# Optimization experiments

Measured on AMD Instinct MI355X. Metric: run time of the kernel, lower is better.

The kernel has to match this reference:

```python
import jax, jax.numpy as jnp
import numpy as np

N = 65536   # total nodes
B = 128     # graphs
G = 512     # nodes per graph
E = 65536   # directed edges (before BU flip + self loops)
IN = 512    # in_feats
HID = 64    # hid_feats
OUT = 64    # out_feats
H = 4       # heads (self.K)
NC = 4      # num_class


def _gat(x, src, dst, W, a_src, a_dst, bias, heads, out_ch, concat):
    # PyG GATConv: lin (no bias) -> per-edge LeakyReLU(0.2) attention logits ->
    # softmax over edges grouped by destination -> weighted sum -> +bias.
    n = x.shape[0]
    h = (x @ W).reshape(n, heads, out_ch)            # [N,H,C]
    asrc = (h * a_src).sum(-1)                       # [N,H]
    adst = (h * a_dst).sum(-1)                       # [N,H]
    e = jax.nn.leaky_relu(asrc[src] + adst[dst], 0.2)  # [Etot,H]
    m = jax.ops.segment_max(e, dst, num_segments=n)
    m = jnp.where(jnp.isfinite(m), m, 0.0)
    ex = jnp.exp(e - m[dst])
    den = jax.ops.segment_sum(ex, dst, num_segments=n)
    alpha = ex / den[dst]                            # self-loops guarantee den>0
    out = jax.ops.segment_sum(alpha[:, :, None] * h[src], dst, num_segments=n)
    out = out.reshape(n, heads * out_ch) if concat else out.mean(1)
    return out + bias


def _smean(v, seg, nseg):
    s = jax.ops.segment_sum(v, seg, num_segments=nseg)
    c = jax.ops.segment_sum(jnp.ones((v.shape[0], 1), v.dtype), seg, num_segments=nseg)
    return s / jnp.maximum(c, 1.0)


def setup_inputs() -> dict:
    key = jax.random.key(0)
    ks = jax.random.split(key, 24)
    x = jax.random.normal(ks[0], (N, IN), jnp.float32)
    root = jax.random.normal(ks[1], (B, IN), jnp.float32)
    # edges kept within each graph of G contiguous nodes (PyG batching layout)
    gid = jax.random.randint(ks[2], (E,), 0, B)
    src = gid * G + jax.random.randint(ks[3], (E,), 0, G)
    dst = gid * G + jax.random.randint(ks[4], (E,), 0, G)
    edge_index = jnp.stack([src, dst]).astype(jnp.int32)
    batch = jnp.repeat(jnp.arange(B, dtype=jnp.int32), G)
    ptr = jnp.arange(B + 1, dtype=jnp.int32) * G
    s = 0.05
    r = lambda i, shp: jax.random.normal(ks[i], shp, jnp.float32) * s
    return {
        'x': x, 'root': root, 'edge_index': edge_index, 'batch': batch, 'ptr': ptr,
        'W_post1': r(5, (IN, HID)), 'W_claim1': r(6, (IN, HID)),
        'W1': r(7, (2 * HID, H * HID)), 'att_src1': r(8, (H, HID)),
        'att_dst1': r(9, (H, HID)), 'b1': r(10, (H * HID,)),
        'W_post2': r(11, (HID, HID)), 'W_claim2': r(12, (IN, HID)),
        'W2': r(13, (8 * HID, H * OUT)), 'att_src2': r(14, (H, OUT)),
        'att_dst2': r(15, (H, OUT)), 'b2': r(16, (OUT,)),
        'W_fc': r(17, (4 * OUT, OUT)), 'b_fc': r(18, (OUT,)),
        'W_clf': r(19, (2 * OUT, NC)), 'b_clf': r(20, (NC,)),
    }


def reference(x, root, edge_index, batch, ptr,
              W_post1, W_claim1, W1, att_src1, att_dst1, b1,
              W_post2, W_claim2, W2, att_src2, att_dst2, b2,
              W_fc, b_fc, W_clf, b_clf):
    n = x.shape[0]
    nb = root.shape[0]
    # merged edges: TD + BU (flipped), then self loops (add_self_loops=True)
    merged = jnp.concatenate([edge_index, edge_index[::-1]], axis=1)
    loops = jnp.arange(n, dtype=edge_index.dtype)
    ei = jnp.concatenate([merged, jnp.stack([loops, loops])], axis=1)
    src, dst = ei[0], ei[1]
    # root broadcast (replaces per-batch python loop)
    root_extend = root[batch]                         # [N,IN]
    # PostLevelAttention: gated fusion of node feats and root feats
    h_x = x @ W_post1
    h_c = root_extend @ W_claim1
    g = jax.nn.sigmoid(h_x + h_c)
    h1 = jnp.concatenate([g * h_x + (1 - g) * h_c, h_x], -1)   # [N,2*HID]
    x2 = _gat(h1, src, dst, W1, att_src1, att_dst1, b1, H, HID, True)  # [N,4*HID]
    xr = jax.nn.relu(x2)
    # PostLevelAttention2 on each of the K=4 head slices (vectorized over k)
    hs = jnp.einsum('nkh,hd->nkd', xr.reshape(n, H, HID), W_post2)  # [N,4,HID]
    hc2 = (root_extend @ W_claim2)[:, None, :]                      # [N,1,HID]
    g2 = jax.nn.sigmoid(hs + hc2)
    x3 = jnp.concatenate([g2 * hs + (1 - g2) * hc2, hs], -1).reshape(n, 8 * HID)
    x4 = _gat(x3, src, dst, W2, att_src2, att_dst2, b2, H, OUT, False)  # [N,OUT]
    xr2 = jax.nn.relu(x4)
    # root embedding per graph (x[ptr[i]]) broadcast back to nodes
    h_c3 = xr2[ptr[:-1]][batch]                        # [N,OUT]
    h_joint = jnp.concatenate([h_c3, xr2, xr2 * h_c3, jnp.abs(h_c3 - xr2)], 1)
    beta = jax.nn.softmax(jnp.tanh(h_joint @ W_fc + b_fc), axis=-1)
    s_hat = _smean(beta * xr2, batch, nb)
    s = _smean(xr2, batch, nb)
    logits = jnp.concatenate([s_hat, s], 1) @ W_clf + b_clf
    return jax.nn.log_softmax(logits, axis=1)
```

## Files before the change

kernel.cpp:

```cpp
#include <hip/hip_runtime.h>
#include <math.h>

#define NN   65536
#define BB   128
#define GGR  512
#define EE   65536
#define INF_ 512
#define HIDD 64

typedef __attribute__((ext_vector_type(8))) short bf16x8;
typedef __attribute__((ext_vector_type(4))) float f32x4;
typedef unsigned short ushort_t;
typedef unsigned int uint_t;

static __device__ __forceinline__ float sigmoidf_(float x){ return 1.0f/(1.0f+__expf(-x)); }
static __device__ __forceinline__ float lrelu_(float x){ return x>=0.0f ? x : 0.2f*x; }
static __device__ __forceinline__ float tanhf_(float x){
  float e = __expf(2.f*x);
  return 1.f - 2.f/(e + 1.f);
}

static __device__ __forceinline__ ushort_t f2b(float f){
  union { float f; uint_t u; } v; v.f = f;
  uint_t u = v.u;
  uint_t r = (u + 0x7fffu + ((u >> 16) & 1u)) >> 16;
  return (ushort_t)r;
}
static __device__ __forceinline__ float b2f(uint_t u16){
  union { uint_t u; float f; } v; v.u = u16 << 16; return v.f;
}

__global__ void k_prep(const float* __restrict__ W1, const float* __restrict__ W2,
                       const float* __restrict__ Wp1, const float* __restrict__ Wp2,
                       const float* __restrict__ Wfc,
                       ushort_t* __restrict__ W1t, ushort_t* __restrict__ W2t,
                       ushort_t* __restrict__ Wp1t, ushort_t* __restrict__ Wp2t,
                       ushort_t* __restrict__ Wfct,
                       const float* __restrict__ root, const float* __restrict__ Wc1,
                       const float* __restrict__ Wc2, float* __restrict__ hc1,
                       float* __restrict__ hc2){
  if (blockIdx.x >= 832){
    int b = blockIdx.x - 832;
    int f = threadIdx.x;
    if (f < 64){
      const float* r = root + (size_t)b*INF_;
      float a1 = 0.f, a2 = 0.f;
      for (int k = 0; k < INF_; ++k){
        float rv = r[k];
        a1 = fmaf(rv, Wc1[k*HIDD+f], a1);
        a2 = fmaf(rv, Wc2[k*HIDD+f], a2);
      }
      hc1[b*HIDD+f] = a1; hc2[b*HIDD+f] = a2;
    }
    return;
  }
  int idx = blockIdx.x*256 + threadIdx.x;
  if (idx < 32768){
    int k = idx >> 8, c = idx & 255;
    W1t[(size_t)c*128 + k] = f2b(W1[idx]);
  } else if (idx < 163840){
    int j = idx - 32768; int k = j >> 8, c = j & 255;
    W2t[(size_t)c*512 + k] = f2b(W2[j]);
  } else if (idx < 196608){
    int j = idx - 163840; int k = j >> 6, c = j & 63;
    Wp1t[(size_t)c*512 + k] = f2b(Wp1[j]);
  } else if (idx < 200704){
    int j = idx - 196608; int k = j >> 6, c = j & 63;
    Wp2t[(size_t)c*64 + k] = f2b(Wp2[j]);
  } else if (idx < 212992){
    int j = idx - 200704; int k = j >> 6, c = j & 63;
    Wfct[(size_t)c*192 + k] = f2b(Wfc[4096 + j]);
  }
}

__global__ __launch_bounds__(256) void k_l1(
    const float* __restrict__ x,
    const ushort_t* __restrict__ Wp1t,
    const float* __restrict__ hc1,
    const ushort_t* __restrict__ W1t,
    const float* __restrict__ att_s, const float* __restrict__ att_d,
    ushort_t* __restrict__ Hout,
    float* __restrict__ asrc, float* __restrict__ adst){
  __shared__ __align__(16) char Hc[16384];
  int tid = threadIdx.x;
  int w = tid >> 6, lane = tid & 63;
  int lr = lane & 15, lk = lane >> 4;
  int n0 = blockIdx.x * 64;
  int g = n0 >> 9;
  int sw = (lr & 7) << 4;
  f32x4 accA[4];
  #pragma unroll
  for (int ci = 0; ci < 4; ++ci) accA[ci] = (f32x4){0.f,0.f,0.f,0.f};
  const char* xrow = (const char*)x + (size_t)(n0 + w*16 + lr)*2048 + lk*32;
  const ushort_t* BbA = Wp1t + (size_t)lr*512 + lk*8;
  #pragma unroll
  for (int j = 0; j < 16; ++j){
    float4 a0 = *(const float4*)(xrow + j*128);
    float4 a1 = *(const float4*)(xrow + j*128 + 16);
    bf16x8 af;
    af[0]=(short)f2b(a0.x); af[1]=(short)f2b(a0.y); af[2]=(short)f2b(a0.z); af[3]=(short)f2b(a0.w);
    af[4]=(short)f2b(a1.x); af[5]=(short)f2b(a1.y); af[6]=(short)f2b(a1.z); af[7]=(short)f2b(a1.w);
    #pragma unroll
    for (int ci = 0; ci < 4; ++ci){
      bf16x8 bfv = *(const bf16x8*)(BbA + (size_t)ci*16*512 + j*32);
      accA[ci] = __builtin_amdgcn_mfma_f32_16x16x32_bf16(af, bfv, accA[ci], 0, 0, 0);
    }
  }
  #pragma unroll
  for (int ci = 0; ci < 4; ++ci){
    int col = ci*16 + lr;
    float hc = hc1[g*64 + col];
    #pragma unroll
    for (int q = 0; q < 4; ++q){
      int row = w*16 + lk*4 + q;
      int swr = (row & 7) << 4;
      float hx = accA[ci][q];
      float gg = sigmoidf_(hx + hc);
      float fo = gg*hx + (1.f-gg)*hc;
      *(ushort_t*)(Hc + ((row*256 + col*2) ^ swr))        = f2b(fo);
      *(ushort_t*)(Hc + ((row*256 + (64 + col)*2) ^ swr)) = f2b(hx);
    }
  }
  __syncthreads();
  int c0 = w * 64;
  f32x4 acc[4][4];
  #pragma unroll
  for (int ri = 0; ri < 4; ++ri)
    #pragma unroll
    for (int ci = 0; ci < 4; ++ci) acc[ri][ci] = (f32x4){0.f,0.f,0.f,0.f};
  #pragma unroll
  for (int k0 = 0; k0 < 128; k0 += 32){
    bf16x8 af[4], bfv[4];
    #pragma unroll
    for (int ri = 0; ri < 4; ++ri){
      int lg = (ri*16 + lr)*256 + (k0 + lk*8)*2;
      af[ri] = *(const bf16x8*)(Hc + (lg ^ sw));
    }
    #pragma unroll
    for (int ci = 0; ci < 4; ++ci)
      bfv[ci] = *(const bf16x8*)(W1t + (size_t)(c0 + ci*16 + lr)*128 + k0 + lk*8);
    #pragma unroll
    for (int ri = 0; ri < 4; ++ri)
      #pragma unroll
      for (int ci = 0; ci < 4; ++ci)
        acc[ri][ci] = __builtin_amdgcn_mfma_f32_16x16x32_bf16(af[ri], bfv[ci], acc[ri][ci], 0, 0, 0);
  }
  float as_[4], ad_[4];
  #pragma unroll
  for (int ci = 0; ci < 4; ++ci){
    as_[ci] = att_s[c0 + ci*16 + lr];
    ad_[ci] = att_d[c0 + ci*16 + lr];
  }
  #pragma unroll
  for (int ri = 0; ri < 4; ++ri){
    #pragma unroll
    for (int q = 0; q < 4; ++q){
      int row = n0 + ri*16 + lk*4 + q;
      float ps = 0.f, pd = 0.f;
      #pragma unroll
      for (int ci = 0; ci < 4; ++ci){
        float v = acc[ri][ci][q];
        Hout[(size_t)row*256 + c0 + ci*16 + lr] = f2b(v);
        ps = fmaf(v, as_[ci], ps);
        pd = fmaf(v, ad_[ci], pd);
      }
      #pragma unroll
      for (int m = 1; m < 16; m <<= 1){
        ps += __shfl_xor(ps, m);
        pd += __shfl_xor(pd, m);
      }
      if (lr == 0){
        asrc[(size_t)row*4 + w] = ps;
        adst[(size_t)row*4 + w] = pd;
      }
    }
  }
}

__global__ __launch_bounds__(256) void k_l2(
    const ushort_t* __restrict__ xrb,
    const ushort_t* __restrict__ Wp2t,
    const float* __restrict__ hc2,
    const ushort_t* __restrict__ W2t,
    const float* __restrict__ att_s, const float* __restrict__ att_d,
    ushort_t* __restrict__ Hout,
    float* __restrict__ asrc, float* __restrict__ adst){
  __shared__ __align__(16) ushort_t x3s[64*128];
  int tid = threadIdx.x;
  int w = tid >> 6, lane = tid & 63;
  int lr = lane & 15, lk = lane >> 4;
  int n0 = blockIdx.x * 64;
  int g = n0 >> 9;
  int sw = (lr & 7) << 4;
  char* Sc = (char*)x3s;
  const ushort_t* Ab = xrb + (size_t)(n0 + w*16 + lr)*256 + lk*8;
  int c0 = w * 64;
  f32x4 acc[4][4];
  #pragma unroll
  for (int ri = 0; ri < 4; ++ri)
    #pragma unroll
    for (int ci = 0; ci < 4; ++ci) acc[ri][ci] = (f32x4){0.f,0.f,0.f,0.f};
  for (int hd = 0; hd < 4; ++hd){
    f32x4 acc2[4];
    #pragma unroll
    for (int ci = 0; ci < 4; ++ci) acc2[ci] = (f32x4){0.f,0.f,0.f,0.f};
    #pragma unroll
    for (int k0 = 0; k0 < 64; k0 += 32){
      bf16x8 af = *(const bf16x8*)(Ab + hd*64 + k0);
      #pragma unroll
      for (int ci = 0; ci < 4; ++ci){
        bf16x8 bfv = *(const bf16x8*)(Wp2t + (size_t)(ci*16 + lr)*64 + k0 + lk*8);
        acc2[ci] = __builtin_amdgcn_mfma_f32_16x16x32_bf16(af, bfv, acc2[ci], 0, 0, 0);
      }
    }
    #pragma unroll
    for (int ci = 0; ci < 4; ++ci){
      int col = ci*16 + lr;
      float hc = hc2[g*64 + col];
      #pragma unroll
      for (int q = 0; q < 4; ++q){
        int row = w*16 + lk*4 + q;
        int swr = (row & 7) << 4;
        float a = acc2[ci][q];
        float gg = sigmoidf_(a + hc);
        *(ushort_t*)(Sc + ((row*256 + col*2) ^ swr))        = f2b(gg*a + (1.f-gg)*hc);
        *(ushort_t*)(Sc + ((row*256 + (64 + col)*2) ^ swr)) = f2b(a);
      }
    }
    __syncthreads();
    #pragma unroll
    for (int k0 = 0; k0 < 128; k0 += 32){
      bf16x8 af[4], bfv[4];
      #pragma unroll
      for (int ri = 0; ri < 4; ++ri){
        int lg = (ri*16 + lr)*256 + (k0 + lk*8)*2;
        af[ri] = *(const bf16x8*)(Sc + (lg ^ sw));
      }
      #pragma unroll
      for (int ci = 0; ci < 4; ++ci)
        bfv[ci] = *(const bf16x8*)(W2t + (size_t)(c0 + ci*16 + lr)*512 + hd*128 + k0 + lk*8);
      #pragma unroll
      for (int ri = 0; ri < 4; ++ri)
        #pragma unroll
        for (int ci = 0; ci < 4; ++ci)
          acc[ri][ci] = __builtin_amdgcn_mfma_f32_16x16x32_bf16(af[ri], bfv[ci], acc[ri][ci], 0, 0, 0);
    }
    if (hd < 3) __syncthreads();
  }
  float as_[4], ad_[4];
  #pragma unroll
  for (int ci = 0; ci < 4; ++ci){
    as_[ci] = att_s[c0 + ci*16 + lr];
    ad_[ci] = att_d[c0 + ci*16 + lr];
  }
  #pragma unroll
  for (int ri = 0; ri < 4; ++ri){
    #pragma unroll
    for (int q = 0; q < 4; ++q){
      int row = n0 + ri*16 + lk*4 + q;
      float ps = 0.f, pd = 0.f;
      #pragma unroll
      for (int ci = 0; ci < 4; ++ci){
        float v = acc[ri][ci][q];
        Hout[(size_t)row*256 + c0 + ci*16 + lr] = f2b(v);
        ps = fmaf(v, as_[ci], ps);
        pd = fmaf(v, ad_[ci], pd);
      }
      #pragma unroll
      for (int m = 1; m < 16; m <<= 1){
        ps += __shfl_xor(ps, m);
        pd += __shfl_xor(pd, m);
      }
      if (lr == 0){
        asrc[(size_t)row*4 + w] = ps;
        adst[(size_t)row*4 + w] = pd;
      }
    }
  }
}

__global__ void k_count(const int* __restrict__ ei, int* __restrict__ deg){
  int t = blockIdx.x*256 + threadIdx.x;
  int s = ei[t], d = ei[EE + t];
  atomicAdd(&deg[d], 1);
  atomicAdd(&deg[s], 1);
}

__global__ void k_scan1(const int* __restrict__ deg, int* __restrict__ offa,
                        int* __restrict__ bsum){
  __shared__ int sm[256];
  int tid = threadIdx.x, idx = blockIdx.x*256 + tid;
  int v = deg[idx] + 1;
  sm[tid] = v; __syncthreads();
  for (int o = 1; o < 256; o <<= 1){
    int t = (tid >= o) ? sm[tid-o] : 0;
    __syncthreads();
    sm[tid] += t;
    __syncthreads();
  }
  offa[idx] = sm[tid] - v;
  if (tid == 255) bsum[blockIdx.x] = sm[255];
}

__global__ void k_scan2(int* __restrict__ bsum){
  __shared__ int sm[256];
  int tid = threadIdx.x;
  int v = bsum[tid];
  sm[tid] = v; __syncthreads();
  for (int o = 1; o < 256; o <<= 1){
    int t = (tid >= o) ? sm[tid-o] : 0;
    __syncthreads();
    sm[tid] += t;
    __syncthreads();
  }
  bsum[tid] = sm[tid] - v;
}

__global__ void k_scan3(int* __restrict__ offa, const int* __restrict__ bsum){
  int idx = blockIdx.x*256 + threadIdx.x;
  offa[idx] += bsum[idx >> 8];
}

__global__ void k_fill(const int* __restrict__ ei, const int* __restrict__ offa,
                       int* __restrict__ cur, int* __restrict__ elist){
  int t = blockIdx.x*256 + threadIdx.x;
  int s = ei[t], d = ei[EE + t];
  int p = atomicAdd(&cur[d], 1); elist[offa[d] + p] = s;
  p = atomicAdd(&cur[s], 1);     elist[offa[s] + p] = d;
  p = atomicAdd(&cur[t], 1);     elist[offa[t] + p] = t;
}

template<int LAYER>
__global__ __launch_bounds__(256) void k_agg(const int* __restrict__ offa,
                                             const int* __restrict__ deg,
                                             const int* __restrict__ elist,
                                             const ushort_t* __restrict__ h,
                                             const float* __restrict__ asrc,
                                             const float* __restrict__ adst,
                                             const float* __restrict__ bias,
                                             ushort_t* __restrict__ outb,
                                             float* __restrict__ outf){
  __shared__ float eS[4][4][17][4];
  __shared__ int   sS[4][4][17];
  int bid = blockIdx.x;
  int swz = (bid & 7) * (4096/8) + (bid >> 3);
  int tid = threadIdx.x;
  int wave = tid >> 6, lane = tid & 63;
  int grp = lane >> 4, l = lane & 15;
  int n = swz*16 + wave*4 + grp;
  int o0 = offa[n], cnt = deg[n] + 1;
  float4 adv = *(const float4*)&adst[(size_t)n*4];
  float ad[4] = {adv.x, adv.y, adv.z, adv.w};
  int lim = (cnt < 16) ? cnt : 16;
  int s_l = elist[o0 + ((l < cnt) ? l : 0)];
  float4 asv = *(const float4*)&asrc[(size_t)s_l*4];
  float e_l[4];
  e_l[0] = lrelu_(asv.x + ad[0]); e_l[1] = lrelu_(asv.y + ad[1]);
  e_l[2] = lrelu_(asv.z + ad[2]); e_l[3] = lrelu_(asv.w + ad[3]);
  if (l < lim){
    sS[wave][grp][l] = s_l;
    *(float4*)&eS[wave][grp][l][0] = make_float4(e_l[0], e_l[1], e_l[2], e_l[3]);
  }
  float m[4];
  #pragma unroll
  for (int hh = 0; hh < 4; ++hh) m[hh] = (l < cnt) ? e_l[hh] : -1e30f;
  for (int i = 16 + l; i < cnt; i += 16){
    int s = elist[o0 + i];
    float4 a2 = *(const float4*)&asrc[(size_t)s*4];
    m[0] = fmaxf(m[0], lrelu_(a2.x + ad[0]));
    m[1] = fmaxf(m[1], lrelu_(a2.y + ad[1]));
    m[2] = fmaxf(m[2], lrelu_(a2.z + ad[2]));
    m[3] = fmaxf(m[3], lrelu_(a2.w + ad[3]));
  }
  #pragma unroll
  for (int mask = 1; mask < 16; mask <<= 1)
    #pragma unroll
    for (int hh = 0; hh < 4; ++hh) m[hh] = fmaxf(m[hh], __shfl_xor(m[hh], mask));
  int myh = l >> 2;
  float mm = m[myh];
  float den = 0.f;
  float accv[16] = {};
  for (int i = 0; i < lim; ++i){
    int s = sS[wave][grp][i];
    float e = eS[wave][grp][i][myh];
    float ex = __expf(e - mm);
    den += ex;
    const uint4* hp = (const uint4*)(h + (size_t)s*256 + l*16);
    uint4 h0 = hp[0], h1v = hp[1];
    uint_t uu[8] = {h0.x, h0.y, h0.z, h0.w, h1v.x, h1v.y, h1v.z, h1v.w};
    #pragma unroll
    for (int r = 0; r < 8; ++r){
      accv[2*r+0] = fmaf(ex, b2f(uu[r] & 0xffffu), accv[2*r+0]);
      accv[2*r+1] = fmaf(ex, b2f(uu[r] >> 16),     accv[2*r+1]);
    }
  }
  for (int i = 16; i < cnt; ++i){
    int s = elist[o0 + i];
    float4 a2 = *(const float4*)&asrc[(size_t)s*4];
    float e = lrelu_(((const float*)&a2)[myh] + ad[myh]);
    float ex = __expf(e - mm);
    den += ex;
    const uint4* hp = (const uint4*)(h + (size_t)s*256 + l*16);
    uint4 h0 = hp[0], h1v = hp[1];
    uint_t uu[8] = {h0.x, h0.y, h0.z, h0.w, h1v.x, h1v.y, h1v.z, h1v.w};
    #pragma unroll
    for (int r = 0; r < 8; ++r){
      accv[2*r+0] = fmaf(ex, b2f(uu[r] & 0xffffu), accv[2*r+0]);
      accv[2*r+1] = fmaf(ex, b2f(uu[r] >> 16),     accv[2*r+1]);
    }
  }
  float inv = 1.0f / den;
  if (LAYER == 1){
    #pragma unroll
    for (int r = 0; r < 4; ++r){
      int c = l*16 + r*4;
      float4 bv = *(const float4*)&bias[c];
      float o0v = fmaxf(accv[r*4+0]*inv + bv.x, 0.f);
      float o1v = fmaxf(accv[r*4+1]*inv + bv.y, 0.f);
      float o2v = fmaxf(accv[r*4+2]*inv + bv.z, 0.f);
      float o3v = fmaxf(accv[r*4+3]*inv + bv.w, 0.f);
      uint2 pk;
      pk.x = (uint_t)f2b(o0v) | ((uint_t)f2b(o1v) << 16);
      pk.y = (uint_t)f2b(o2v) | ((uint_t)f2b(o3v) << 16);
      *(uint2*)&outb[(size_t)n*256 + c] = pk;
    }
  } else {
    #pragma unroll
    for (int r = 0; r < 16; ++r) accv[r] *= inv;
    #pragma unroll
    for (int r = 0; r < 16; ++r){
      accv[r] += __shfl_xor(accv[r], 4);
      accv[r] += __shfl_xor(accv[r], 8);
    }
    if (l < 4){
      #pragma unroll
      for (int r = 0; r < 4; ++r){
        int c = l*16 + r*4;
        float4 bv = *(const float4*)&bias[c];
        float4 o;
        o.x = fmaxf(accv[r*4+0]*0.25f + bv.x, 0.f);
        o.y = fmaxf(accv[r*4+1]*0.25f + bv.y, 0.f);
        o.z = fmaxf(accv[r*4+2]*0.25f + bv.z, 0.f);
        o.w = fmaxf(accv[r*4+3]*0.25f + bv.w, 0.f);
        *(float4*)&outf[(size_t)n*64 + c] = o;
      }
    }
  }
}

__global__ __launch_bounds__(256) void k_pool_mfma(
    const float* __restrict__ xr2,
    const ushort_t* __restrict__ Wfct,
    const float* __restrict__ Wfc,
    const float* __restrict__ bfc,
    float* __restrict__ shat,
    float* __restrict__ ssum){
  __shared__ __align__(16) float xs[64][68];
  __shared__ float rls[64];
  __shared__ float bs[64];
  __shared__ float ls_sh[64];
  __shared__ float ls_s[64];
  int tid = threadIdx.x;
  int n0 = blockIdx.x * 64;
  int g = n0 >> 9;
  {
    int row = tid >> 4, col4 = (tid & 15) * 4;
    #pragma unroll
    for (int i = 0; i < 4; ++i){
      float4 v = *(const float4*)&xr2[(size_t)(n0 + row + i*16)*64 + col4];
      *(float4*)&xs[row + i*16][col4] = v;
    }
    if (tid < 16){
      float4 v = *(const float4*)&xr2[(size_t)((size_t)g*GGR)*64 + tid*4];
      *(float4*)&rls[tid*4] = v;
    }
    if (tid >= 128 && tid < 192){ ls_sh[tid-128] = 0.f; ls_s[tid-128] = 0.f; }
  }
  __syncthreads();
  if (tid < 64){
    float b = bfc[tid];
    for (int j = 0; j < 64; ++j) b = fmaf(rls[j], Wfc[j*64 + tid], b);
    bs[tid] = b;
  }
  __syncthreads();
  int w = tid >> 6, lane = tid & 63;
  int lr = lane & 15, lk = lane >> 4;
  f32x4 acc[4];
  #pragma unroll
  for (int ci = 0; ci < 4; ++ci) acc[ci] = (f32x4){0.f,0.f,0.f,0.f};
  int arow = w*16 + lr;
  #pragma unroll
  for (int k0 = 0; k0 < 192; k0 += 32){
    int seg = k0 >> 6;
    int cb = (k0 & 63) + lk*8;
    bf16x8 af;
    #pragma unroll
    for (int j = 0; j < 8; ++j){
      float xv = xs[arow][cb + j];
      float rv = rls[cb + j];
      float v = (seg == 0) ? xv : (seg == 1 ? xv*rv : fabsf(rv - xv));
      af[j] = (short)f2b(v);
    }
    #pragma unroll
    for (int ci = 0; ci < 4; ++ci){
      bf16x8 bfv = *(const bf16x8*)(Wfct + (size_t)(ci*16+lr)*192 + k0 + lk*8);
      acc[ci] = __builtin_amdgcn_mfma_f32_16x16x32_bf16(af, bfv, acc[ci], 0, 0, 0);
    }
  }
  float bsv[4];
  #pragma unroll
  for (int ci = 0; ci < 4; ++ci) bsv[ci] = bs[ci*16 + lr];
  float c_sh[4] = {0.f,0.f,0.f,0.f}, c_s[4] = {0.f,0.f,0.f,0.f};
  #pragma unroll
  for (int q = 0; q < 4; ++q){
    int rrow = w*16 + lk*4 + q;
    float t[4];
    float mx = -1e30f;
    #pragma unroll
    for (int ci = 0; ci < 4; ++ci){
      t[ci] = tanhf_(acc[ci][q] + bsv[ci]);
      mx = fmaxf(mx, t[ci]);
    }
    #pragma unroll
    for (int mask = 1; mask < 16; mask <<= 1) mx = fmaxf(mx, __shfl_xor(mx, mask));
    float e[4], s = 0.f;
    #pragma unroll
    for (int ci = 0; ci < 4; ++ci){ e[ci] = __expf(t[ci] - mx); s += e[ci]; }
    #pragma unroll
    for (int mask = 1; mask < 16; mask <<= 1) s += __shfl_xor(s, mask);
    float invs = 1.0f / s;
    #pragma unroll
    for (int ci = 0; ci < 4; ++ci){
      float xv = xs[rrow][ci*16 + lr];
      c_sh[ci] = fmaf(e[ci]*invs, xv, c_sh[ci]);
      c_s[ci] += xv;
    }
  }
  #pragma unroll
  for (int ci = 0; ci < 4; ++ci){
    c_sh[ci] += __shfl_xor(c_sh[ci], 16); c_sh[ci] += __shfl_xor(c_sh[ci], 32);
    c_s[ci]  += __shfl_xor(c_s[ci], 16);  c_s[ci]  += __shfl_xor(c_s[ci], 32);
  }
  if (lk == 0){
    #pragma unroll
    for (int ci = 0; ci < 4; ++ci){
      atomicAdd(&ls_sh[ci*16 + lr], c_sh[ci]);
      atomicAdd(&ls_s[ci*16 + lr], c_s[ci]);
    }
  }
  __syncthreads();
  if (tid < 64){
    atomicAdd(&shat[g*64 + tid], ls_sh[tid]);
    atomicAdd(&ssum[g*64 + tid], ls_s[tid]);
  }
}

__global__ void k_final(const float* __restrict__ shat, const float* __restrict__ ssum,
                        const float* __restrict__ Wc, const float* __restrict__ bc,
                        float* __restrict__ outp){
  int g = threadIdx.x;
  float l0 = bc[0], l1 = bc[1], l2 = bc[2], l3 = bc[3];
  const float s512 = 1.0f/512.0f;
  for (int j = 0; j < 64; ++j){
    float sh = shat[g*64 + j]*s512;
    float ss = ssum[g*64 + j]*s512;
    float4 w1 = *(const float4*)&Wc[j*4];
    float4 w2 = *(const float4*)&Wc[(64+j)*4];
    l0 = fmaf(sh, w1.x, fmaf(ss, w2.x, l0));
    l1 = fmaf(sh, w1.y, fmaf(ss, w2.y, l1));
    l2 = fmaf(sh, w1.z, fmaf(ss, w2.z, l2));
    l3 = fmaf(sh, w1.w, fmaf(ss, w2.w, l3));
  }
  float mx = fmaxf(fmaxf(l0,l1), fmaxf(l2,l3));
  float s = __expf(l0-mx)+__expf(l1-mx)+__expf(l2-mx)+__expf(l3-mx);
  float lse = mx + logf(s);
  outp[g*4+0] = l0 - lse;
  outp[g*4+1] = l1 - lse;
  outp[g*4+2] = l2 - lse;
  outp[g*4+3] = l3 - lse;
}

extern "C" void kernel_launch(void* const* d_in, const int* in_sizes, int n_in,
                              void* d_out, int out_size, void* d_ws, size_t ws_size,
                              hipStream_t stream){
  const float* x        = (const float*)d_in[0];
  const float* root     = (const float*)d_in[1];
  const int*   ei       = (const int*)d_in[2];
  const float* W_post1  = (const float*)d_in[5];
  const float* W_claim1 = (const float*)d_in[6];
  const float* W1       = (const float*)d_in[7];
  const float* att_src1 = (const float*)d_in[8];
  const float* att_dst1 = (const float*)d_in[9];
  const float* b1       = (const float*)d_in[10];
  const float* W_post2  = (const float*)d_in[11];
  const float* W_claim2 = (const float*)d_in[12];
  const float* W2       = (const float*)d_in[13];
  const float* att_src2 = (const float*)d_in[14];
  const float* att_dst2 = (const float*)d_in[15];
  const float* b2       = (const float*)d_in[16];
  const float* W_fc     = (const float*)d_in[17];
  const float* b_fc     = (const float*)d_in[18];
  const float* W_clf    = (const float*)d_in[19];
  const float* b_clf    = (const float*)d_in[20];
  float* out = (float*)d_out;

  char* w = (char*)d_ws;
  size_t o = 0;
  auto alloc = [&](size_t bytes)->char*{ char* p = w + o; o += (bytes + 255) & ~(size_t)255; return p; };
  ushort_t* RB   = (ushort_t*)alloc((size_t)NN*256*2);
  ushort_t* xrb  = (ushort_t*)alloc((size_t)NN*256*2);
  float* xr2  = (float*)alloc((size_t)NN*64*4);
  float* asrc = (float*)alloc((size_t)NN*4*4);
  float* adst = (float*)alloc((size_t)NN*4*4);
  float* hc1  = (float*)alloc(128*64*4);
  float* hc2  = (float*)alloc(128*64*4);
  ushort_t* W1t  = (ushort_t*)alloc((size_t)256*128*2);
  ushort_t* W2t  = (ushort_t*)alloc((size_t)256*512*2);
  ushort_t* Wp1t = (ushort_t*)alloc((size_t)64*512*2);
  ushort_t* Wp2t = (ushort_t*)alloc((size_t)64*64*2);
  ushort_t* Wfct = (ushort_t*)alloc((size_t)64*192*2);
  int*   deg  = (int*)alloc((size_t)NN*4);
  int*   cur  = (int*)alloc((size_t)NN*4);
  int*   offa = (int*)alloc((size_t)NN*4);
  int*   bsum = (int*)alloc(256*4);
  int*   elist= (int*)alloc((size_t)(2*EE+NN)*4);
  float* shat = (float*)alloc(128*64*4);
  float* ssumv= (float*)alloc(128*64*4);

  ushort_t* h2b = RB;
  ushort_t* h3b = RB;

  hipMemsetAsync(deg,  0, (size_t)NN*8, stream);
  hipMemsetAsync(shat, 0, 2*128*64*4, stream);

  k_prep<<<960, 256, 0, stream>>>(W1, W2, W_post1, W_post2, W_fc,
                                  W1t, W2t, Wp1t, Wp2t, Wfct,
                                  root, W_claim1, W_claim2, hc1, hc2);
  k_count<<<256, 256, 0, stream>>>(ei, deg);
  k_scan1<<<256, 256, 0, stream>>>(deg, offa, bsum);
  k_scan2<<<1, 256, 0, stream>>>(bsum);
  k_scan3<<<256, 256, 0, stream>>>(offa, bsum);
  k_fill<<<256, 256, 0, stream>>>(ei, offa, cur, elist);
  k_l1<<<1024, 256, 0, stream>>>(x, Wp1t, hc1, W1t, att_src1, att_dst1, h2b, asrc, adst);
  k_agg<1><<<4096, 256, 0, stream>>>(offa, deg, elist, h2b, asrc, adst, b1, xrb, nullptr);
  k_l2<<<1024, 256, 0, stream>>>(xrb, Wp2t, hc2, W2t, att_src2, att_dst2, h3b, asrc, adst);
  k_agg<2><<<4096, 256, 0, stream>>>(offa, deg, elist, h3b, asrc, adst, b2, nullptr, xr2);
  k_pool_mfma<<<1024, 256, 0, stream>>>(xr2, Wfct, W_fc, b_fc, shat, ssumv);
  k_final<<<1, 128, 0, stream>>>(shat, ssumv, W_clf, b_clf, out);
  (void)in_sizes; (void)n_in; (void)out_size; (void)ws_size;
}
```

Measured before the change: 245.3 us.

## Fuse layer-1 GAT aggregation into layer-2 projection kernel via shared memory

The layer-1 attention aggregation (softmax over incoming edges plus bias and ReLU) now runs inside the layer-2 GEMM kernel. Each block aggregates its 64 nodes into a swizzled LDS tile and feeds that tile straight to the MFMA projections, so the 32 MB bf16 xrb intermediate is never written to or read back from global memory, and one launch disappears. Separate buffers for h2/h3 and the layer-2 attention scalars are added so the fused kernel can read layer-1 data while writing layer-2 outputs. In exchange, the fused kernel uses about 48 KB of LDS per block, which can lower occupancy, and only 1024 blocks now do the gather work that was previously spread over 4096.

New measurement: 291.0 us. +18.6%, slower.

```diff
diff --git a/kernel.cpp b/kernel.cpp
--- a/kernel.cpp
+++ b/kernel.cpp
@@ -177,24 +177,114 @@
   }
 }
 
-__global__ __launch_bounds__(256) void k_l2(
-    const ushort_t* __restrict__ xrb,
+__global__ __launch_bounds__(256) void k_al2(
+    const int* __restrict__ offa, const int* __restrict__ deg,
+    const int* __restrict__ elist,
+    const ushort_t* __restrict__ h,
+    const float* __restrict__ asrc1, const float* __restrict__ adst1,
+    const float* __restrict__ b1,
     const ushort_t* __restrict__ Wp2t,
     const float* __restrict__ hc2,
     const ushort_t* __restrict__ W2t,
     const float* __restrict__ att_s, const float* __restrict__ att_d,
     ushort_t* __restrict__ Hout,
-    float* __restrict__ asrc, float* __restrict__ adst){
-  __shared__ __align__(16) ushort_t x3s[64*128];
+    float* __restrict__ asrc2, float* __restrict__ adst2){
+  __shared__ __align__(16) char Xs[32768];
+  __shared__ __align__(16) char Sc[16384];
+  float* eS = (float*)Sc;
+  int*   sS = (int*)(Sc + 8192);
   int tid = threadIdx.x;
-  int w = tid >> 6, lane = tid & 63;
+  int bid = blockIdx.x;
+  int swzb = (bid & 7) * 128 + (bid >> 3);
+  int n0 = swzb * 64;
+  int g = n0 >> 9;
+  int wv = tid >> 6, lane = tid & 63;
+  int grp = lane >> 4, l = lane & 15;
   int lr = lane & 15, lk = lane >> 4;
-  int n0 = blockIdx.x * 64;
-  int g = n0 >> 9;
   int sw = (lr & 7) << 4;
-  char* Sc = (char*)x3s;
-  const ushort_t* Ab = xrb + (size_t)(n0 + w*16 + lr)*256 + lk*8;
-  int c0 = w * 64;
+  for (int it = 0; it < 4; ++it){
+    int row = wv*16 + it*4 + grp;
+    int n = n0 + row;
+    int o0 = offa[n], cnt = deg[n] + 1;
+    float4 adv = *(const float4*)&adst1[(size_t)n*4];
+    float ad[4] = {adv.x, adv.y, adv.z, adv.w};
+    int lim = (cnt < 16) ? cnt : 16;
+    int s_l = elist[o0 + ((l < cnt) ? l : 0)];
+    float4 asv = *(const float4*)&asrc1[(size_t)s_l*4];
+    float e_l[4];
+    e_l[0] = lrelu_(asv.x + ad[0]); e_l[1] = lrelu_(asv.y + ad[1]);
+    e_l[2] = lrelu_(asv.z + ad[2]); e_l[3] = lrelu_(asv.w + ad[3]);
+    int slot = wv*4 + grp;
+    if (l < lim){
+      sS[slot*17 + l] = s_l;
+      *(float4*)&eS[(slot*17 + l)*4] = make_float4(e_l[0], e_l[1], e_l[2], e_l[3]);
+    }
+    float m[4];
+    #pragma unroll
+    for (int hh = 0; hh < 4; ++hh) m[hh] = (l < cnt) ? e_l[hh] : -1e30f;
+    for (int i = 16 + l; i < cnt; i += 16){
+      int s = elist[o0 + i];
+      float4 a2 = *(const float4*)&asrc1[(size_t)s*4];
+      m[0] = fmaxf(m[0], lrelu_(a2.x + ad[0]));
+      m[1] = fmaxf(m[1], lrelu_(a2.y + ad[1]));
+      m[2] = fmaxf(m[2], lrelu_(a2.z + ad[2]));
+      m[3] = fmaxf(m[3], lrelu_(a2.w + ad[3]));
+    }
+    #pragma unroll
+    for (int mask = 1; mask < 16; mask <<= 1)
+      #pragma unroll
+      for (int hh = 0; hh < 4; ++hh) m[hh] = fmaxf(m[hh], __shfl_xor(m[hh], mask));
+    int myh = l >> 2;
+    float mm = m[myh];
+    float den = 0.f;
+    float accv[16] = {};
+    for (int i = 0; i < lim; ++i){
+      int s = sS[slot*17 + i];
+      float e = eS[(slot*17 + i)*4 + myh];
+      float ex = __expf(e - mm);
+      den += ex;
+      const uint4* hp = (const uint4*)(h + (size_t)s*256 + l*16);
+      uint4 h0 = hp[0], h1v = hp[1];
+      uint_t uu[8] = {h0.x, h0.y, h0.z, h0.w, h1v.x, h1v.y, h1v.z, h1v.w};
+      #pragma unroll
+      for (int r = 0; r < 8; ++r){
+        accv[2*r+0] = fmaf(ex, b2f(uu[r] & 0xffffu), accv[2*r+0]);
+        accv[2*r+1] = fmaf(ex, b2f(uu[r] >> 16),     accv[2*r+1]);
+      }
+    }
+    for (int i = 16; i < cnt; ++i){
+      int s = elist[o0 + i];
+      float4 a2 = *(const float4*)&asrc1[(size_t)s*4];
+      float e = lrelu_(((const float*)&a2)[myh] + ad[myh]);
+      float ex = __expf(e - mm);
+      den += ex;
+      const uint4* hp = (const uint4*)(h + (size_t)s*256 + l*16);
+      uint4 h0 = hp[0], h1v = hp[1];
+      uint_t uu[8] = {h0.x, h0.y, h0.z, h0.w, h1v.x, h1v.y, h1v.z, h1v.w};
+      #pragma unroll
+      for (int r = 0; r < 8; ++r){
+        accv[2*r+0] = fmaf(ex, b2f(uu[r] & 0xffffu), accv[2*r+0]);
+        accv[2*r+1] = fmaf(ex, b2f(uu[r] >> 16),     accv[2*r+1]);
+      }
+    }
+    float inv = 1.0f / den;
+    int swr = (row & 7) << 4;
+    #pragma unroll
+    for (int r = 0; r < 4; ++r){
+      int c = l*16 + r*4;
+      float4 bv = *(const float4*)&b1[c];
+      float o0v = fmaxf(accv[r*4+0]*inv + bv.x, 0.f);
+      float o1v = fmaxf(accv[r*4+1]*inv + bv.y, 0.f);
+      float o2v = fmaxf(accv[r*4+2]*inv + bv.z, 0.f);
+      float o3v = fmaxf(accv[r*4+3]*inv + bv.w, 0.f);
+      uint2 pk;
+      pk.x = (uint_t)f2b(o0v) | ((uint_t)f2b(o1v) << 16);
+      pk.y = (uint_t)f2b(o2v) | ((uint_t)f2b(o3v) << 16);
+      *(uint2*)(Xs + ((row*512 + c*2) ^ swr)) = pk;
+    }
+  }
+  __syncthreads();
+  int c0 = wv * 64;
   f32x4 acc[4][4];
   #pragma unroll
   for (int ri = 0; ri < 4; ++ri)
@@ -206,7 +296,8 @@
     for (int ci = 0; ci < 4; ++ci) acc2[ci] = (f32x4){0.f,0.f,0.f,0.f};
     #pragma unroll
     for (int k0 = 0; k0 < 64; k0 += 32){
-      bf16x8 af = *(const bf16x8*)(Ab + hd*64 + k0);
+      int lg = (wv*16 + lr)*512 + (hd*64 + k0 + lk*8)*2;
+      bf16x8 af = *(const bf16x8*)(Xs + (lg ^ sw));
       #pragma unroll
       for (int ci = 0; ci < 4; ++ci){
         bf16x8 bfv = *(const bf16x8*)(Wp2t + (size_t)(ci*16 + lr)*64 + k0 + lk*8);
@@ -219,7 +310,7 @@
       float hc = hc2[g*64 + col];
       #pragma unroll
       for (int q = 0; q < 4; ++q){
-        int row = w*16 + lk*4 + q;
+        int row = wv*16 + lk*4 + q;
         int swr = (row & 7) << 4;
         float a = acc2[ci][q];
         float gg = sigmoidf_(a + hc);
@@ -272,8 +363,8 @@
         pd += __shfl_xor(pd, m);
       }
       if (lr == 0){
-        asrc[(size_t)row*4 + w] = ps;
-        adst[(size_t)row*4 + w] = pd;
+        asrc2[(size_t)row*4 + wv] = ps;
+        adst2[(size_t)row*4 + wv] = pd;
       }
     }
   }
@@ -330,16 +421,14 @@
   p = atomicAdd(&cur[t], 1);     elist[offa[t] + p] = t;
 }
 
-template<int LAYER>
-__global__ __launch_bounds__(256) void k_agg(const int* __restrict__ offa,
-                                             const int* __restrict__ deg,
-                                             const int* __restrict__ elist,
-                                             const ushort_t* __restrict__ h,
-                                             const float* __restrict__ asrc,
-                                             const float* __restrict__ adst,
-                                             const float* __restrict__ bias,
-                                             ushort_t* __restrict__ outb,
-                                             float* __restrict__ outf){
+__global__ __launch_bounds__(256) void k_agg2(const int* __restrict__ offa,
+                                              const int* __restrict__ deg,
+                                              const int* __restrict__ elist,
+                                              const ushort_t* __restrict__ h,
+                                              const float* __restrict__ asrc,
+                                              const float* __restrict__ adst,
+                                              const float* __restrict__ bias,
+                                              float* __restrict__ outf){
   __shared__ float eS[4][4][17][4];
   __shared__ int   sS[4][4][17];
   int bid = blockIdx.x;
@@ -410,40 +499,24 @@
     }
   }
   float inv = 1.0f / den;
-  if (LAYER == 1){
+  #pragma unroll
+  for (int r = 0; r < 16; ++r) accv[r] *= inv;
+  #pragma unroll
+  for (int r = 0; r < 16; ++r){
+    accv[r] += __shfl_xor(accv[r], 4);
+    accv[r] += __shfl_xor(accv[r], 8);
+  }
+  if (l < 4){
     #pragma unroll
     for (int r = 0; r < 4; ++r){
       int c = l*16 + r*4;
       float4 bv = *(const float4*)&bias[c];
-      float o0v = fmaxf(accv[r*4+0]*inv + bv.x, 0.f);
-      float o1v = fmaxf(accv[r*4+1]*inv + bv.y, 0.f);
-      float o2v = fmaxf(accv[r*4+2]*inv + bv.z, 0.f);
-      float o3v = fmaxf(accv[r*4+3]*inv + bv.w, 0.f);
-      uint2 pk;
-      pk.x = (uint_t)f2b(o0v) | ((uint_t)f2b(o1v) << 16);
-      pk.y = (uint_t)f2b(o2v) | ((uint_t)f2b(o3v) << 16);
-      *(uint2*)&outb[(size_t)n*256 + c] = pk;
-    }
-  } else {
-    #pragma unroll
-    for (int r = 0; r < 16; ++r) accv[r] *= inv;
-    #pragma unroll
-    for (int r = 0; r < 16; ++r){
-      accv[r] += __shfl_xor(accv[r], 4);
-      accv[r] += __shfl_xor(accv[r], 8);
-    }
-    if (l < 4){
-      #pragma unroll
-      for (int r = 0; r < 4; ++r){
-        int c = l*16 + r*4;
-        float4 bv = *(const float4*)&bias[c];
-        float4 o;
-        o.x = fmaxf(accv[r*4+0]*0.25f + bv.x, 0.f);
-        o.y = fmaxf(accv[r*4+1]*0.25f + bv.y, 0.f);
-        o.z = fmaxf(accv[r*4+2]*0.25f + bv.z, 0.f);
-        o.w = fmaxf(accv[r*4+3]*0.25f + bv.w, 0.f);
-        *(float4*)&outf[(size_t)n*64 + c] = o;
-      }
+      float4 o;
+      o.x = fmaxf(accv[r*4+0]*0.25f + bv.x, 0.f);
+      o.y = fmaxf(accv[r*4+1]*0.25f + bv.y, 0.f);
+      o.z = fmaxf(accv[r*4+2]*0.25f + bv.z, 0.f);
+      o.w = fmaxf(accv[r*4+3]*0.25f + bv.w, 0.f);
+      *(float4*)&outf[(size_t)n*64 + c] = o;
     }
   }
 }
@@ -607,11 +680,13 @@
   char* w = (char*)d_ws;
   size_t o = 0;
   auto alloc = [&](size_t bytes)->char*{ char* p = w + o; o += (bytes + 255) & ~(size_t)255; return p; };
-  ushort_t* RB   = (ushort_t*)alloc((size_t)NN*256*2);
-  ushort_t* xrb  = (ushort_t*)alloc((size_t)NN*256*2);
-  float* xr2  = (float*)alloc((size_t)NN*64*4);
-  float* asrc = (float*)alloc((size_t)NN*4*4);
-  float* adst = (float*)alloc((size_t)NN*4*4);
+  ushort_t* h2b  = (ushort_t*)alloc((size_t)NN*256*2);
+  ushort_t* h3b  = (ushort_t*)alloc((size_t)NN*256*2);
+  float* xr2   = (float*)alloc((size_t)NN*64*4);
+  float* asrc  = (float*)alloc((size_t)NN*4*4);
+  float* adst  = (float*)alloc((size_t)NN*4*4);
+  float* asrc2 = (float*)alloc((size_t)NN*4*4);
+  float* adst2 = (float*)alloc((size_t)NN*4*4);
   float* hc1  = (float*)alloc(128*64*4);
   float* hc2  = (float*)alloc(128*64*4);
   ushort_t* W1t  = (ushort_t*)alloc((size_t)256*128*2);
@@ -627,9 +702,6 @@
   float* shat = (float*)alloc(128*64*4);
   float* ssumv= (float*)alloc(128*64*4);
 
-  ushort_t* h2b = RB;
-  ushort_t* h3b = RB;
-
   hipMemsetAsync(deg,  0, (size_t)NN*8, stream);
   hipMemsetAsync(shat, 0, 2*128*64*4, stream);
 
@@ -642,9 +714,10 @@
   k_scan3<<<256, 256, 0, stream>>>(offa, bsum);
   k_fill<<<256, 256, 0, stream>>>(ei, offa, cur, elist);
   k_l1<<<1024, 256, 0, stream>>>(x, Wp1t, hc1, W1t, att_src1, att_dst1, h2b, asrc, adst);
-  k_agg<1><<<4096, 256, 0, stream>>>(offa, deg, elist, h2b, asrc, adst, b1, xrb, nullptr);
-  k_l2<<<1024, 256, 0, stream>>>(xrb, Wp2t, hc2, W2t, att_src2, att_dst2, h3b, asrc, adst);
-  k_agg<2><<<4096, 256, 0, stream>>>(offa, deg, elist, h3b, asrc, adst, b2, nullptr, xr2);
+  k_al2<<<1024, 256, 0, stream>>>(offa, deg, elist, h2b, asrc, adst, b1,
+                                  Wp2t, hc2, W2t, att_src2, att_dst2,
+                                  h3b, asrc2, adst2);
+  k_agg2<<<4096, 256, 0, stream>>>(offa, deg, elist, h3b, asrc2, adst2, b2, xr2);
   k_pool_mfma<<<1024, 256, 0, stream>>>(xr2, Wfct, W_fc, b_fc, shat, ssumv);
   k_final<<<1, 128, 0, stream>>>(shat, ssumv, W_clf, b_clf, out);
   (void)in_sizes; (void)n_in; (void)out_size; (void)ws_size;
```
